# Performance work log

Hardware: AMD Instinct MI355X
Metric: run time of the kernel (lower is better)

## Reference

```python
import jax, jax.numpy as jnp
import numpy as np

B, S, D, C, H = 4, 2048, 1024, 2, 16
LN_EPS = 1e-5


def setup_inputs() -> dict:
    key = jax.random.key(0)
    ks = jax.random.split(key, 6)
    return {
        "token_emb": jax.random.normal(ks[0], (B, S, D), dtype=jnp.float32),
        "chunk_w": jax.random.normal(ks[1], (D, C * D), dtype=jnp.float32) * 0.02,
        "chunk_b": jnp.zeros((D,), dtype=jnp.float32),
        "in_proj_w": jax.random.normal(ks[2], (3 * D, D), dtype=jnp.float32) * 0.02,
        "in_proj_b": jnp.zeros((3 * D,), dtype=jnp.float32),
        "out_proj_w": jax.random.normal(ks[3], (D, D), dtype=jnp.float32) * 0.02,
        "out_proj_b": jnp.zeros((D,), dtype=jnp.float32),
        "ln_g": jnp.ones((D,), dtype=jnp.float32),
        "ln_b": jnp.zeros((D,), dtype=jnp.float32),
        "num_heads": H,
    }


def _layer_norm(x, g, b):
    mu = jnp.mean(x, axis=-1, keepdims=True)
    var = jnp.mean((x - mu) ** 2, axis=-1, keepdims=True)
    return (x - mu) * jax.lax.rsqrt(var + LN_EPS) * g + b


def reference(token_emb, chunk_w, chunk_b, in_proj_w, in_proj_b,
              out_proj_w, out_proj_b, ln_g, ln_b, num_heads):
    Bq, Sq, Dq = token_emb.shape
    c = chunk_w.shape[1] // Dq
    # Sliding windows with zero padding at the end (vectorized unfold).
    padded = jnp.pad(token_emb, ((0, 0), (0, c - 1), (0, 0)))
    # (B, S, c*D): concat the c shifted views along feature dim
    windows = jnp.concatenate([padded[:, k:k + Sq, :] for k in range(c)], axis=-1)
    chunk = jnp.einsum('bsf,df->bsd', windows, chunk_w) + chunk_b  # (B,S,D)

    # Multi-head self-attention (torch nn.MultiheadAttention semantics).
    qkv = jnp.einsum('bsd,ed->bse', chunk, in_proj_w) + in_proj_b
    q, k, v = jnp.split(qkv, 3, axis=-1)
    dh = Dq // num_heads
    q = q.reshape(Bq, Sq, num_heads, dh)
    k = k.reshape(Bq, Sq, num_heads, dh)
    v = v.reshape(Bq, Sq, num_heads, dh)
    scores = jnp.einsum('bqhd,bkhd->bhqk', q, k) / jnp.sqrt(jnp.float32(dh))
    probs = jax.nn.softmax(scores, axis=-1)
    attn = jnp.einsum('bhqk,bkhd->bqhd', probs, v).reshape(Bq, Sq, Dq)
    attn = jnp.einsum('bsd,ed->bse', attn, out_proj_w) + out_proj_b

    return _layer_norm(chunk + attn, ln_g, ln_b)
```

## Files before the change

### kernel.cpp

```cpp
#include <hip/hip_runtime.h>


typedef __bf16 bf16x8 __attribute__((ext_vector_type(8)));
typedef float f32x4 __attribute__((ext_vector_type(4)));
typedef float f32x16 __attribute__((ext_vector_type(16)));

#if __has_builtin(__builtin_amdgcn_exp2f)
#define EXP2(x) __builtin_amdgcn_exp2f(x)
#else
#define EXP2(x) exp2f(x)
#endif

__device__ __forceinline__ unsigned short f2bf(float x) {
  unsigned u = __float_as_uint(x);
  u += 0x7fffu + ((u >> 16) & 1u);
  return (unsigned short)(u >> 16);
}

__device__ __forceinline__ void glds16(const ushort* g, ushort* l) {
  __builtin_amdgcn_global_load_lds(
      (const __attribute__((address_space(1))) unsigned int*)g,
      (__attribute__((address_space(3))) unsigned int*)l, 16, 0, 0);
}

__global__ __launch_bounds__(256) void build_awin(const float* __restrict__ emb,
                                                  ushort* __restrict__ aw) {
  const int i = blockIdx.x * 256 + threadIdx.x;
  const int e = i * 4;
  const int m = e >> 11;
  const int k = e & 2047;
  float4 v;
  if (k < 1024) {
    v = *(const float4*)(emb + (size_t)m * 1024 + k);
  } else {
    const int s = m & 2047;
    if (s == 2047) v = make_float4(0.f, 0.f, 0.f, 0.f);
    else           v = *(const float4*)(emb + (size_t)(m + 1) * 1024 + (k - 1024));
  }
  ushort4 o;
  o.x = f2bf(v.x); o.y = f2bf(v.y); o.z = f2bf(v.z); o.w = f2bf(v.w);
  *(ushort4*)(aw + (size_t)e) = o;
}

__global__ __launch_bounds__(256) void cvt_bf16(const float* __restrict__ in,
                                                ushort* __restrict__ out, int n4) {
  const int i = blockIdx.x * 256 + threadIdx.x;
  if (i >= n4) return;
  float4 v = ((const float4*)in)[i];
  ushort4 o;
  o.x = f2bf(v.x); o.y = f2bf(v.y); o.z = f2bf(v.z); o.w = f2bf(v.w);
  ((ushort4*)out)[i] = o;
}

__global__ __launch_bounds__(256) void gemm_bt(
    const ushort* __restrict__ A, const ushort* __restrict__ W,
    const float* __restrict__ bias, int M, int N, int K, int mode,
    float* __restrict__ outf, ushort* __restrict__ outb,
    const float* __restrict__ resid) {
  __shared__ __align__(16) ushort sA[4096];
  __shared__ __align__(16) ushort sB[4096];
  const int t = threadIdx.x, wave = t >> 6, lane = t & 63;
  const int c16 = lane & 15, quad = lane >> 4;
  const int wm = wave >> 1, wn = wave & 1;
  const int m0 = blockIdx.y * 128, n0 = blockIdx.x * 128;
  f32x4 acc[4][4] = {};
  const int rowa = (wave & 1) * 64 + lane;
  const int ks = wave >> 1;
  const ushort* gA0 = A + (size_t)(m0 + rowa) * K + ks * 8;
  const ushort* gA1 = gA0 + 16;
  const ushort* gB0 = W + (size_t)(n0 + rowa) * K + ks * 8;
  const ushort* gB1 = gB0 + 16;
  ushort* lA0 = sA + wave * 512;
  ushort* lA1 = sA + (wave + 4) * 512;
  ushort* lB0 = sB + wave * 512;
  ushort* lB1 = sB + (wave + 4) * 512;
  for (int k0 = 0; k0 < K; k0 += 32) {
    __syncthreads();
    glds16(gA0 + k0, lA0);
    glds16(gA1 + k0, lA1);
    glds16(gB0 + k0, lB0);
    glds16(gB1 + k0, lB1);
    __syncthreads();
    bf16x8 af[4], bfr[4];
#pragma unroll
    for (int i = 0; i < 4; ++i) {
      af[i]  = *(const bf16x8*)(sA + (quad * 128 + wm * 64 + i * 16 + c16) * 8);
      bfr[i] = *(const bf16x8*)(sB + (quad * 128 + wn * 64 + i * 16 + c16) * 8);
    }
#pragma unroll
    for (int mt = 0; mt < 4; ++mt)
#pragma unroll
      for (int nt = 0; nt < 4; ++nt)
        acc[mt][nt] = __builtin_amdgcn_mfma_f32_16x16x32_bf16(af[mt], bfr[nt],
                                                              acc[mt][nt], 0, 0, 0);
  }
  float bv[4];
#pragma unroll
  for (int nt = 0; nt < 4; ++nt) bv[nt] = bias[n0 + wn * 64 + nt * 16 + c16];
#pragma unroll
  for (int mt = 0; mt < 4; ++mt) {
#pragma unroll
    for (int nt = 0; nt < 4; ++nt) {
      const int n = n0 + wn * 64 + nt * 16 + c16;
#pragma unroll
      for (int r = 0; r < 4; ++r) {
        const int m = m0 + wm * 64 + mt * 16 + quad * 4 + r;
        const size_t idx = (size_t)m * N + n;
        float v = acc[mt][nt][r] + bv[nt];
        if (mode == 0)      { outf[idx] = v; outb[idx] = f2bf(v); }
        else if (mode == 1) { outb[idx] = f2bf(v); }
        else                { outf[idx] = v + resid[idx]; }
      }
    }
  }
}

__global__ __launch_bounds__(256) void vtrans(const ushort* __restrict__ qkv,
                                              ushort* __restrict__ vt) {
  const int sb = blockIdx.x, h = blockIdx.y, b = blockIdx.z;
  __shared__ ushort tile[64][72];
  const int t = threadIdx.x;
  {
    const int row = t >> 3, c8 = (t & 7) * 8;
    const ushort* src = qkv + (size_t)(b * 2048 + sb * 64 + row) * 3072 + 2048 + h * 64 + c8;
    *(uint4*)&tile[row][c8]      = *(const uint4*)src;
    *(uint4*)&tile[row + 32][c8] = *(const uint4*)(src + 32 * 3072);
  }
  __syncthreads();
  const int d = t >> 2, seg = (t & 3) * 16;
  unsigned wbuf[8];
#pragma unroll
  for (int i = 0; i < 8; ++i)
    wbuf[i] = (unsigned)tile[seg + 2 * i][d] | ((unsigned)tile[seg + 2 * i + 1][d] << 16);
  ushort* dst = vt + (size_t)((b * 16 + h) * 64 + d) * 2048 + sb * 64 + seg;
  *(uint4*)(dst)     = *(uint4*)&wbuf[0];
  *(uint4*)(dst + 8) = *(uint4*)&wbuf[4];
}

__global__ __launch_bounds__(256) void attn_kernel(
    const ushort* __restrict__ qkv, const ushort* __restrict__ vtp,
    ushort* __restrict__ attn_out) {
  const int S = 2048;
  const int qblk = blockIdx.x, h = blockIdx.y, b = blockIdx.z;
  const int t = threadIdx.x, wave = t >> 6, lane = t & 63;
  const int c32 = lane & 31, hi = lane >> 5;
  __shared__ __align__(16) ushort sK[8192];
  __shared__ __align__(16) ushort sV[8192];
  __shared__ __align__(16) ushort sP[4][4096];
  const int q0 = qblk * 128;
  const size_t qrow = (size_t)(b * S + q0 + wave * 32 + c32);
  bf16x8 qf[4];
  {
    const ushort* qp = qkv + qrow * 3072 + h * 64 + hi * 8;
#pragma unroll
    for (int dk = 0; dk < 4; ++dk) qf[dk] = *(const bf16x8*)(qp + dk * 16);
  }
  f32x16 o0 = {}, o1 = {};
  float mi = -1e30f, li = 0.f;
  const float k1 = 0.18033688011112042f;
  ushort* sPw = &sP[wave][0];
  const int j0 = wave * 4;

  for (int kv0 = 0; kv0 < S; kv0 += 128) {
    __syncthreads();
#pragma unroll
    for (int c = 0; c < 4; ++c) {
      const int j = j0 + c;
      const int dslot = j >> 1, key = (j & 1) * 64 + lane;
      glds16(qkv + (size_t)(b * S + kv0 + key) * 3072 + 1024 + h * 64 + dslot * 8,
             sK + j * 512);
      const int d = j * 4 + (lane >> 4);
      const int ksv = (lane & 15) ^ (d & 15);
      glds16(vtp + (size_t)((b * 16 + h) * 64 + d) * S + kv0 + ksv * 8,
             sV + j * 512);
    }
    __syncthreads();
    f32x16 sc[4];
#pragma unroll
    for (int kt = 0; kt < 4; ++kt) {
      f32x16 z = {};
#pragma unroll
      for (int dk = 0; dk < 4; ++dk) {
        bf16x8 kf = *(const bf16x8*)(sK + ((dk * 2 + hi) * 128 + kt * 32 + c32) * 8);
        z = __builtin_amdgcn_mfma_f32_32x32x16_bf16(kf, qf[dk], z, 0, 0, 0);
      }
      sc[kt] = z;
    }
    float mx = sc[0][0];
#pragma unroll
    for (int kt = 0; kt < 4; ++kt)
#pragma unroll
      for (int r = 0; r < 16; ++r) mx = fmaxf(mx, sc[kt][r]);
    mx = fmaxf(mx, __shfl_xor(mx, 32));
    const float mn = fmaxf(mi, mx * k1);
    const float alpha = EXP2(mi - mn);
    float sum = 0.f;
#pragma unroll
    for (int kt = 0; kt < 4; ++kt)
#pragma unroll
      for (int r = 0; r < 16; ++r) {
        const float p = EXP2(sc[kt][r] * k1 - mn);
        sc[kt][r] = p;
        sum += p;
      }
    sum += __shfl_xor(sum, 32);
    li = li * alpha + sum;
    mi = mn;
    o0 *= alpha;
    o1 *= alpha;
#pragma unroll
    for (int kt = 0; kt < 4; ++kt)
#pragma unroll
      for (int g = 0; g < 4; ++g) {
        uint2 w2;
        w2.x = __builtin_amdgcn_perm(__float_as_uint(sc[kt][g * 4 + 1]),
                                     __float_as_uint(sc[kt][g * 4 + 0]), 0x07060302u);
        w2.y = __builtin_amdgcn_perm(__float_as_uint(sc[kt][g * 4 + 3]),
                                     __float_as_uint(sc[kt][g * 4 + 2]), 0x07060302u);
        const int ksp = (kt * 4 + g) ^ (c32 & 15);
        *(uint2*)(sPw + c32 * 128 + ksp * 8 + hi * 4) = w2;
      }
#pragma unroll
    for (int kc = 0; kc < 8; ++kc) {
      const int ksq = (kc * 2 + hi);
      bf16x8 pf = *(const bf16x8*)(sPw + c32 * 128 + (ksq ^ (c32 & 15)) * 8);
      bf16x8 vf0 = *(const bf16x8*)(sV + (c32 * 16 + (ksq ^ (c32 & 15))) * 8);
      o0 = __builtin_amdgcn_mfma_f32_32x32x16_bf16(vf0, pf, o0, 0, 0, 0);
      bf16x8 vf1 = *(const bf16x8*)(sV + ((32 + c32) * 16 + (ksq ^ (c32 & 15))) * 8);
      o1 = __builtin_amdgcn_mfma_f32_32x32x16_bf16(vf1, pf, o1, 0, 0, 0);
    }
  }
  const float inv = 1.f / li;
  ushort* orow = attn_out + qrow * 1024 + h * 64;
#pragma unroll
  for (int dt = 0; dt < 2; ++dt) {
    const f32x16 ov = dt ? o1 : o0;
#pragma unroll
    for (int g = 0; g < 4; ++g) {
      float v0 = ov[g * 4 + 0] * inv, v1 = ov[g * 4 + 1] * inv;
      float v2 = ov[g * 4 + 2] * inv, v3 = ov[g * 4 + 3] * inv;
      uint2 w2;
      w2.x = (unsigned)f2bf(v0) | ((unsigned)f2bf(v1) << 16);
      w2.y = (unsigned)f2bf(v2) | ((unsigned)f2bf(v3) << 16);
      *(uint2*)(orow + dt * 32 + g * 8 + hi * 4) = w2;
    }
  }
}

__global__ __launch_bounds__(256) void ln_kernel(const float* __restrict__ y,
                                                 const float* __restrict__ g,
                                                 const float* __restrict__ bta,
                                                 float* __restrict__ out) {
  const int m = blockIdx.x;
  const int t = threadIdx.x;
  const float* row = y + (size_t)m * 1024;
  float4 v = ((const float4*)row)[t];
  float s = v.x + v.y + v.z + v.w;
  float s2 = v.x * v.x + v.y * v.y + v.z * v.z + v.w * v.w;
#pragma unroll
  for (int off = 1; off < 64; off <<= 1) {
    s += __shfl_xor(s, off, 64);
    s2 += __shfl_xor(s2, off, 64);
  }
  __shared__ float red[8];
  const int wave = t >> 6, lane = t & 63;
  if (lane == 0) { red[wave] = s; red[4 + wave] = s2; }
  __syncthreads();
  s = red[0] + red[1] + red[2] + red[3];
  s2 = red[4] + red[5] + red[6] + red[7];
  const float mu = s * (1.f / 1024.f);
  const float var = s2 * (1.f / 1024.f) - mu * mu;
  const float rs = rsqrtf(var + 1e-5f);
  float4 gg = ((const float4*)g)[t];
  float4 bb = ((const float4*)bta)[t];
  float4 o;
  o.x = (v.x - mu) * rs * gg.x + bb.x;
  o.y = (v.y - mu) * rs * gg.y + bb.y;
  o.z = (v.z - mu) * rs * gg.z + bb.z;
  o.w = (v.w - mu) * rs * gg.w + bb.w;
  ((float4*)(out + (size_t)m * 1024))[t] = o;
}

extern "C" void kernel_launch(void* const* d_in, const int* in_sizes, int n_in,
                              void* d_out, int out_size, void* d_ws, size_t ws_size,
                              hipStream_t stream) {
  const float* emb        = (const float*)d_in[0];
  const float* chunk_w    = (const float*)d_in[1];
  const float* chunk_b    = (const float*)d_in[2];
  const float* in_proj_w  = (const float*)d_in[3];
  const float* in_proj_b  = (const float*)d_in[4];
  const float* out_proj_w = (const float*)d_in[5];
  const float* out_proj_b = (const float*)d_in[6];
  const float* ln_g       = (const float*)d_in[7];
  const float* ln_b       = (const float*)d_in[8];

  char* w = (char*)d_ws;
  const size_t MBy = (size_t)1 << 20;
  ushort* qkvb  = (ushort*)(w + 0);
  ushort* awin  = (ushort*)(w + 0);
  float*  y     = (float*)(w + 0);
  float*  chunkf = (float*)(w + 48 * MBy);
  ushort* chunkb = (ushort*)(w + 80 * MBy);
  ushort* vtb    = (ushort*)(w + 96 * MBy);
  ushort* attnb  = (ushort*)(w + 112 * MBy);
  ushort* cwb    = (ushort*)(w + 128 * MBy);
  ushort* ipwb   = (ushort*)(w + 132 * MBy);
  ushort* opwb   = (ushort*)(w + 138 * MBy);

  build_awin<<<16384, 256, 0, stream>>>(emb, awin);
  cvt_bf16<<<2048, 256, 0, stream>>>(chunk_w, cwb, 2 * 1024 * 1024 / 4);
  cvt_bf16<<<3072, 256, 0, stream>>>(in_proj_w, ipwb, 3 * 1024 * 1024 / 4);
  cvt_bf16<<<1024, 256, 0, stream>>>(out_proj_w, opwb, 1024 * 1024 / 4);

  gemm_bt<<<dim3(1024 / 128, 8192 / 128), 256, 0, stream>>>(
      awin, cwb, chunk_b, 8192, 1024, 2048, 0, chunkf, chunkb, nullptr);

  gemm_bt<<<dim3(3072 / 128, 8192 / 128), 256, 0, stream>>>(
      chunkb, ipwb, in_proj_b, 8192, 3072, 1024, 1, nullptr, qkvb, nullptr);

  vtrans<<<dim3(32, 16, 4), 256, 0, stream>>>(qkvb, vtb);

  attn_kernel<<<dim3(2048 / 128, 16, 4), 256, 0, stream>>>(qkvb, vtb, attnb);

  gemm_bt<<<dim3(1024 / 128, 8192 / 128), 256, 0, stream>>>(
      attnb, opwb, out_proj_b, 8192, 1024, 1024, 2, y, nullptr, chunkf);

  ln_kernel<<<8192, 256, 0, stream>>>(y, ln_g, ln_b, (float*)d_out);
}
```

Before: 513.0 us.

## Deepen GEMM K-step to 64 and stream P through a small per-wave LDS slice

The GEMM now stages 64 K-elements per barrier pair instead of 32, so each tile pays half as many synchronizations and issues more loads per round. This doubles the GEMM's LDS footprint. The attention kernel now converts and consumes P one 32-key slice at a time through a 1 KB-per-wave buffer instead of materializing the full 128-key P tile, which cuts LDS from 64 KB to about 40 KB and may allow more resident blocks. The V and P swizzles change to an XOR of row bits to avoid bank conflicts under the new layout.

```diff
diff --git a/kernel.cpp b/kernel.cpp
--- a/kernel.cpp
+++ b/kernel.cpp
@@ -57,42 +57,49 @@
     const float* __restrict__ bias, int M, int N, int K, int mode,
     float* __restrict__ outf, ushort* __restrict__ outb,
     const float* __restrict__ resid) {
-  __shared__ __align__(16) ushort sA[4096];
-  __shared__ __align__(16) ushort sB[4096];
+  __shared__ __align__(16) ushort sA[8192];
+  __shared__ __align__(16) ushort sB[8192];
   const int t = threadIdx.x, wave = t >> 6, lane = t & 63;
   const int c16 = lane & 15, quad = lane >> 4;
   const int wm = wave >> 1, wn = wave & 1;
   const int m0 = blockIdx.y * 128, n0 = blockIdx.x * 128;
   f32x4 acc[4][4] = {};
-  const int rowa = (wave & 1) * 64 + lane;
-  const int ks = wave >> 1;
-  const ushort* gA0 = A + (size_t)(m0 + rowa) * K + ks * 8;
-  const ushort* gA1 = gA0 + 16;
-  const ushort* gB0 = W + (size_t)(n0 + rowa) * K + ks * 8;
-  const ushort* gB1 = gB0 + 16;
-  ushort* lA0 = sA + wave * 512;
-  ushort* lA1 = sA + (wave + 4) * 512;
-  ushort* lB0 = sB + wave * 512;
-  ushort* lB1 = sB + (wave + 4) * 512;
-  for (int k0 = 0; k0 < K; k0 += 32) {
+  const ushort* gA[4];
+  const ushort* gB[4];
+  ushort* lA[4];
+  ushort* lB[4];
+#pragma unroll
+  for (int c = 0; c < 4; ++c) {
+    const int j = wave * 4 + c;
+    const int ks = j >> 1, row = (j & 1) * 64 + lane;
+    gA[c] = A + (size_t)(m0 + row) * K + ks * 8;
+    gB[c] = W + (size_t)(n0 + row) * K + ks * 8;
+    lA[c] = sA + j * 512;
+    lB[c] = sB + j * 512;
+  }
+  for (int k0 = 0; k0 < K; k0 += 64) {
     __syncthreads();
-    glds16(gA0 + k0, lA0);
-    glds16(gA1 + k0, lA1);
-    glds16(gB0 + k0, lB0);
-    glds16(gB1 + k0, lB1);
+#pragma unroll
+    for (int c = 0; c < 4; ++c) {
+      glds16(gA[c] + k0, lA[c]);
+      glds16(gB[c] + k0, lB[c]);
+    }
     __syncthreads();
-    bf16x8 af[4], bfr[4];
-#pragma unroll
-    for (int i = 0; i < 4; ++i) {
-      af[i]  = *(const bf16x8*)(sA + (quad * 128 + wm * 64 + i * 16 + c16) * 8);
-      bfr[i] = *(const bf16x8*)(sB + (quad * 128 + wn * 64 + i * 16 + c16) * 8);
-    }
-#pragma unroll
-    for (int mt = 0; mt < 4; ++mt)
-#pragma unroll
-      for (int nt = 0; nt < 4; ++nt)
-        acc[mt][nt] = __builtin_amdgcn_mfma_f32_16x16x32_bf16(af[mt], bfr[nt],
-                                                              acc[mt][nt], 0, 0, 0);
+#pragma unroll
+    for (int kc = 0; kc < 2; ++kc) {
+      bf16x8 af[4], bfr[4];
+#pragma unroll
+      for (int i = 0; i < 4; ++i) {
+        af[i]  = *(const bf16x8*)(sA + ((kc * 4 + quad) * 128 + wm * 64 + i * 16 + c16) * 8);
+        bfr[i] = *(const bf16x8*)(sB + ((kc * 4 + quad) * 128 + wn * 64 + i * 16 + c16) * 8);
+      }
+#pragma unroll
+      for (int mt = 0; mt < 4; ++mt)
+#pragma unroll
+        for (int nt = 0; nt < 4; ++nt)
+          acc[mt][nt] = __builtin_amdgcn_mfma_f32_16x16x32_bf16(af[mt], bfr[nt],
+                                                                acc[mt][nt], 0, 0, 0);
+    }
   }
   float bv[4];
 #pragma unroll
@@ -146,9 +153,13 @@
   const int c32 = lane & 31, hi = lane >> 5;
   __shared__ __align__(16) ushort sK[8192];
   __shared__ __align__(16) ushort sV[8192];
-  __shared__ __align__(16) ushort sP[4][4096];
+  __shared__ __align__(16) ushort sP[4][1024];
   const int q0 = qblk * 128;
   const size_t qrow = (size_t)(b * S + q0 + wave * 32 + c32);
+  const int swq = (c32 ^ (c32 >> 2)) & 3;
+  const int swv0 = (c32 ^ (c32 >> 3)) & 15;
+  const int dv1 = 32 + c32;
+  const int swv1 = (dv1 ^ (dv1 >> 3)) & 15;
   bf16x8 qf[4];
   {
     const ushort* qp = qkv + qrow * 3072 + h * 64 + hi * 8;
@@ -170,7 +181,7 @@
       glds16(qkv + (size_t)(b * S + kv0 + key) * 3072 + 1024 + h * 64 + dslot * 8,
              sK + j * 512);
       const int d = j * 4 + (lane >> 4);
-      const int ksv = (lane & 15) ^ (d & 15);
+      const int ksv = (lane & 15) ^ ((d ^ (d >> 3)) & 15);
       glds16(vtp + (size_t)((b * 16 + h) * 64 + d) * S + kv0 + ksv * 8,
              sV + j * 512);
     }
@@ -209,7 +220,7 @@
     o0 *= alpha;
     o1 *= alpha;
 #pragma unroll
-    for (int kt = 0; kt < 4; ++kt)
+    for (int kt = 0; kt < 4; ++kt) {
 #pragma unroll
       for (int g = 0; g < 4; ++g) {
         uint2 w2;
@@ -217,17 +228,17 @@
                                      __float_as_uint(sc[kt][g * 4 + 0]), 0x07060302u);
         w2.y = __builtin_amdgcn_perm(__float_as_uint(sc[kt][g * 4 + 3]),
                                      __float_as_uint(sc[kt][g * 4 + 2]), 0x07060302u);
-        const int ksp = (kt * 4 + g) ^ (c32 & 15);
-        *(uint2*)(sPw + c32 * 128 + ksp * 8 + hi * 4) = w2;
-      }
-#pragma unroll
-    for (int kc = 0; kc < 8; ++kc) {
-      const int ksq = (kc * 2 + hi);
-      bf16x8 pf = *(const bf16x8*)(sPw + c32 * 128 + (ksq ^ (c32 & 15)) * 8);
-      bf16x8 vf0 = *(const bf16x8*)(sV + (c32 * 16 + (ksq ^ (c32 & 15))) * 8);
-      o0 = __builtin_amdgcn_mfma_f32_32x32x16_bf16(vf0, pf, o0, 0, 0, 0);
-      bf16x8 vf1 = *(const bf16x8*)(sV + ((32 + c32) * 16 + (ksq ^ (c32 & 15))) * 8);
-      o1 = __builtin_amdgcn_mfma_f32_32x32x16_bf16(vf1, pf, o1, 0, 0, 0);
+        *(uint2*)(sPw + c32 * 32 + (g ^ swq) * 8 + hi * 4) = w2;
+      }
+#pragma unroll
+      for (int e = 0; e < 2; ++e) {
+        bf16x8 pf = *(const bf16x8*)(sPw + c32 * 32 + ((2 * e + hi) ^ swq) * 8);
+        const int ks = kt * 4 + e * 2 + hi;
+        bf16x8 vf0 = *(const bf16x8*)(sV + (c32 * 16 + (ks ^ swv0)) * 8);
+        o0 = __builtin_amdgcn_mfma_f32_32x32x16_bf16(vf0, pf, o0, 0, 0, 0);
+        bf16x8 vf1 = *(const bf16x8*)(sV + (dv1 * 16 + (ks ^ swv1)) * 8);
+        o1 = __builtin_amdgcn_mfma_f32_32x32x16_bf16(vf1, pf, o1, 0, 0, 0);
+      }
     }
   }
   const float inv = 1.f / li;
```

Measured after the change: 599.8 us. +16.9%, slower.
